# Kernel tuning notes

Measured on AMD Instinct MI355X. Metric: run time of the kernel, lower is better.

The kernel has to match this reference:

```python
import jax, jax.numpy as jnp
import numpy as np

N_HEADS = 16

def setup_inputs() -> dict:
    key = jax.random.key(0)
    ks = jax.random.split(key, 5)
    d = 2048
    s = 0.02
    return {
        "x": jax.random.normal(ks[0], (1, 2048, d), dtype=jnp.float32),
        "Wq": jax.random.normal(ks[1], (d, d), dtype=jnp.float32) * s,
        "bq": jnp.zeros((d,), jnp.float32),
        "Wk": jax.random.normal(ks[2], (d, d), dtype=jnp.float32) * s,
        "bk": jnp.zeros((d,), jnp.float32),
        "Wv": jax.random.normal(ks[3], (d, d), dtype=jnp.float32) * s,
        "bv": jnp.zeros((d,), jnp.float32),
        "Wo": jax.random.normal(ks[4], (d, d), dtype=jnp.float32) * s,
        "bo": jnp.zeros((d,), jnp.float32),
    }

def reference(x, Wq, bq, Wk, bk, Wv, bv, Wo, bo):
    B, S, D = x.shape
    H = N_HEADS
    dk = D // H
    # QKV projections -> [B, H, S, dk]
    def proj(W, b):
        return (x @ W + b).reshape(B, S, H, dk).transpose(0, 2, 1, 3)
    q, k, v = proj(Wq, bq), proj(Wk, bk), proj(Wv, bv)
    scores = jnp.einsum('bhqd,bhkd->bhqk', q, k) / jnp.sqrt(jnp.float32(dk))
    # _apply_sliding_window_attention: block-reshaped tril == plain causal mask
    causal = jnp.tril(jnp.ones((S, S), dtype=bool))
    scores = jnp.where(causal, scores, -jnp.inf)
    probs = jax.nn.softmax(scores, axis=-1)
    out = jnp.einsum('bhqk,bhkd->bhqd', probs, v)  # [B,H,S,dk]
    out = out.transpose(0, 2, 1, 3).reshape(B, S, D)
    return out @ Wo + bo
```

## Files before the change

kernel.cpp:

```cpp
#include <hip/hip_runtime.h>
#include <hip/hip_bf16.h>
#include <stdint.h>

typedef unsigned short u16;
typedef __attribute__((ext_vector_type(8))) __bf16 bf16x8;
typedef __attribute__((ext_vector_type(4))) float f32x4;

#define LOG2E 1.4426950408889634f

__device__ __forceinline__ float bf2f(u16 u) {
  union { uint32_t u; float f; } v; v.u = ((uint32_t)u) << 16;
  return v.f;
}

__device__ __forceinline__ uint32_t pk2(float a, float b) {
  union { __hip_bfloat162 h; uint32_t u; } x;
  x.h = __float22bfloat162_rn(make_float2(a, b));
  return x.u;
}

__device__ __forceinline__ void gl_lds16(const void* g, void* l) {
  __builtin_amdgcn_global_load_lds((const __attribute__((address_space(1))) void*)g,
                                   (__attribute__((address_space(3))) void*)l,
                                   16, 0, 0);
}

__device__ __forceinline__ f32x4 mfma16(bf16x8 a, bf16x8 b, f32x4 c) {
  return __builtin_amdgcn_mfma_f32_16x16x32_bf16(a, b, c, 0, 0, 0);
}

__global__ void cvt_bf16(const float* __restrict__ src, u16* __restrict__ dst) {
  int i = (blockIdx.x * 256 + threadIdx.x) * 4;
  float4 f = *(const float4*)(src + i);
  uint2 o;
  o.x = pk2(f.x, f.y);
  o.y = pk2(f.z, f.w);
  *(uint2*)(dst + i) = o;
}

__global__ void transpose_cvt(const float* __restrict__ W0, const float* __restrict__ W1,
                              const float* __restrict__ W2, const float* __restrict__ W3,
                              u16* __restrict__ out) {
  __shared__ float tile[64][65];
  int z = blockIdx.z;
  const float* W = (z == 0) ? W0 : (z == 1) ? W1 : (z == 2) ? W2 : W3;
  u16* dst = out + (size_t)z * 2048 * 2048;
  int k0 = blockIdx.y * 64, n0 = blockIdx.x * 64;
  int lx = threadIdx.x & 63, ly = threadIdx.x >> 6;
#pragma unroll
  for (int p = 0; p < 16; ++p) {
    int row = p * 4 + ly;
    tile[row][lx] = W[(size_t)(k0 + row) * 2048 + n0 + lx];
  }
  __syncthreads();
  int kc = threadIdx.x & 7;
  int rbase = threadIdx.x >> 3;
#pragma unroll
  for (int p = 0; p < 2; ++p) {
    int n = rbase + p * 32;
    uint4 o;
    o.x = pk2(tile[kc * 8 + 0][n], tile[kc * 8 + 1][n]);
    o.y = pk2(tile[kc * 8 + 2][n], tile[kc * 8 + 3][n]);
    o.z = pk2(tile[kc * 8 + 4][n], tile[kc * 8 + 5][n]);
    o.w = pk2(tile[kc * 8 + 6][n], tile[kc * 8 + 7][n]);
    *(uint4*)(dst + (size_t)(n0 + n) * 2048 + k0 + kc * 8) = o;
  }
}

__launch_bounds__(256, 2)
__global__ void gemm_bt(const u16* __restrict__ A, const u16* __restrict__ Bt,
                        const float* __restrict__ b0, const float* __restrict__ b1,
                        const float* __restrict__ b2,
                        u16* __restrict__ outQ, u16* __restrict__ outK,
                        u16* __restrict__ outVT) {
  extern __shared__ char smem[];
  u16* As = (u16*)smem;
  u16* Bs = (u16*)(smem + 16384);
  const int K = 2048;
  const int tid = threadIdx.x;
  const int lane = tid & 63, wid = tid >> 6;
  const int c = lane & 15, q = lane >> 4;
  const int wm = wid >> 1, wn = wid & 1;
  const int tm = blockIdx.y, tn = blockIdx.x;
  const size_t Abase = (size_t)tm * 128 * K;
  const size_t Bbase = (size_t)tn * 128 * K;

  f32x4 acc[4][4] = {};

  for (int kt = 0; kt < K / 64; ++kt) {
#pragma unroll
    for (int t = 0; t < 4; ++t) {
      int slot = wid * 256 + t * 64 + lane;
      int row = slot >> 3, cs = slot & 7;
      int cc = cs ^ (row & 7);
      const u16* ga = A + Abase + (size_t)row * K + kt * 64 + cc * 8;
      gl_lds16(ga, (char*)As + (size_t)(wid * 256 + t * 64) * 16);
      const u16* gb = Bt + Bbase + (size_t)row * K + kt * 64 + cc * 8;
      gl_lds16(gb, (char*)Bs + (size_t)(wid * 256 + t * 64) * 16);
    }
    __syncthreads();
#pragma unroll
    for (int kc = 0; kc < 2; ++kc) {
      bf16x8 af[4], bfr[4];
#pragma unroll
      for (int i = 0; i < 4; ++i) {
        int rowa = wm * 64 + i * 16 + c;
        int cha = ((kc << 2) | q) ^ (rowa & 7);
        af[i] = *(const bf16x8*)((const char*)As + rowa * 128 + cha * 16);
        int rowb = wn * 64 + i * 16 + c;
        int chb = ((kc << 2) | q) ^ (rowb & 7);
        bfr[i] = *(const bf16x8*)((const char*)Bs + rowb * 128 + chb * 16);
      }
#pragma unroll
      for (int i = 0; i < 4; ++i)
#pragma unroll
        for (int j = 0; j < 4; ++j)
          acc[i][j] = mfma16(af[i], bfr[j], acc[i][j]);
    }
    __syncthreads();
  }

  int proj = tn >> 4;
  int h = tn & 15;
  const float* bias = (proj == 0) ? b0 : (proj == 1) ? b1 : b2;
  if (proj < 2) {
    u16* out = (proj == 0) ? outQ : outK;
    float scale = (proj == 0) ? 0.08838834764831845f : 1.0f;
#pragma unroll
    for (int i = 0; i < 4; ++i) {
      int s0 = tm * 128 + wm * 64 + i * 16 + q * 4;
#pragma unroll
      for (int j = 0; j < 4; ++j) {
        int d = wn * 64 + j * 16 + c;
        float bv = bias[h * 128 + d];
        uint32_t p01 = pk2((acc[i][j][0] + bv) * scale, (acc[i][j][1] + bv) * scale);
        uint32_t p23 = pk2((acc[i][j][2] + bv) * scale, (acc[i][j][3] + bv) * scale);
        u16* o = out + ((size_t)h * 2048 + s0) * 128 + d;
        o[0]   = (u16)p01;
        o[128] = (u16)(p01 >> 16);
        o[256] = (u16)p23;
        o[384] = (u16)(p23 >> 16);
      }
    }
  } else {
    u16* Cs = (u16*)smem;
#pragma unroll
    for (int i = 0; i < 4; ++i) {
      int sl = wm * 64 + i * 16 + q * 4;
#pragma unroll
      for (int j = 0; j < 4; ++j) {
        int dl = wn * 64 + j * 16 + c;
        float bv = bias[h * 128 + dl];
        uint2 pk;
        pk.x = pk2(acc[i][j][0] + bv, acc[i][j][1] + bv);
        pk.y = pk2(acc[i][j][2] + bv, acc[i][j][3] + bv);
        *(uint2*)(Cs + dl * 136 + sl) = pk;
      }
    }
    __syncthreads();
#pragma unroll
    for (int rr = 0; rr < 8; ++rr) {
      int d = rr * 16 + (tid >> 4);
      int sc = (tid & 15) * 8;
      uint4 vv = *(const uint4*)(Cs + d * 136 + sc);
      *(uint4*)(outVT + ((size_t)(h * 128 + d)) * 2048 + tm * 128 + sc) = vv;
    }
  }
}

__launch_bounds__(256, 2)
__global__ void gemm_op(const u16* __restrict__ A, const u16* __restrict__ Bt,
                        const float* __restrict__ bias, float* __restrict__ out) {
  extern __shared__ char smem[];
  u16* As = (u16*)smem;
  u16* Bs = (u16*)(smem + 16384);
  const int K = 2048;
  const int tid = threadIdx.x;
  const int lane = tid & 63, wid = tid >> 6;
  const int c = lane & 15, q = lane >> 4;
  const int wm = wid >> 1, wn = wid & 1;
  const int tm = blockIdx.y, tn = blockIdx.x;
  const size_t Abase = (size_t)tm * 128 * K;
  const size_t Bbase = (size_t)tn * 64 * K;

  f32x4 acc[4][2] = {};

  for (int kt = 0; kt < K / 64; ++kt) {
#pragma unroll
    for (int t = 0; t < 4; ++t) {
      int slot = wid * 256 + t * 64 + lane;
      int row = slot >> 3, cs = slot & 7;
      int cc = cs ^ (row & 7);
      gl_lds16(A + Abase + (size_t)row * K + kt * 64 + cc * 8,
               (char*)As + (size_t)(wid * 256 + t * 64) * 16);
    }
#pragma unroll
    for (int t = 0; t < 2; ++t) {
      int slot = wid * 128 + t * 64 + lane;
      int row = slot >> 3, cs = slot & 7;
      int cc = cs ^ (row & 7);
      gl_lds16(Bt + Bbase + (size_t)row * K + kt * 64 + cc * 8,
               (char*)Bs + (size_t)(wid * 128 + t * 64) * 16);
    }
    __syncthreads();
#pragma unroll
    for (int kc = 0; kc < 2; ++kc) {
      bf16x8 af[4], bfr[2];
#pragma unroll
      for (int i = 0; i < 4; ++i) {
        int rowa = wm * 64 + i * 16 + c;
        int cha = ((kc << 2) | q) ^ (rowa & 7);
        af[i] = *(const bf16x8*)((const char*)As + rowa * 128 + cha * 16);
      }
#pragma unroll
      for (int j = 0; j < 2; ++j) {
        int rowb = wn * 32 + j * 16 + c;
        int chb = ((kc << 2) | q) ^ (rowb & 7);
        bfr[j] = *(const bf16x8*)((const char*)Bs + rowb * 128 + chb * 16);
      }
#pragma unroll
      for (int i = 0; i < 4; ++i)
#pragma unroll
        for (int j = 0; j < 2; ++j)
          acc[i][j] = mfma16(af[i], bfr[j], acc[i][j]);
    }
    __syncthreads();
  }

#pragma unroll
  for (int i = 0; i < 4; ++i) {
    int rowg = tm * 128 + wm * 64 + i * 16 + q * 4;
#pragma unroll
    for (int j = 0; j < 2; ++j) {
      int colg = tn * 64 + wn * 32 + j * 16 + c;
      float bv = bias[colg];
#pragma unroll
      for (int r = 0; r < 4; ++r)
        out[(size_t)(rowg + r) * 2048 + colg] = acc[i][j][r] + bv;
    }
  }
}

__launch_bounds__(256, 2)
__global__ void attn_kernel(const u16* __restrict__ Qb, const u16* __restrict__ Kb,
                            const u16* __restrict__ Vt,
                            u16* __restrict__ Opb, float* __restrict__ lpb) {
  extern __shared__ char smem[];
  u16* Ks = (u16*)smem;
  u16* Vs = (u16*)(smem + 16384);
  u16* Ps = (u16*)(smem + 32768);
  int b = blockIdx.x;
  int split, qt, h;
  if (b < 256) { split = 0; qt = b >> 4; h = b & 15; }
  else { split = 1; int idx = b - 256; qt = 15 - (idx >> 4); h = idx & 15; }
  u16* Op = Opb + (size_t)split * 4194304;
  float* lp = lpb + (size_t)split * 32768;
  const int ktBase = split ? (qt + 1) : 0;
  const int ntiles = qt + 1;

  const int tid = threadIdx.x, lane = tid & 63, wid = tid >> 6;
  const int c = lane & 15, q = lane >> 4;

  bf16x8 qf[2][4];
#pragma unroll
  for (int i = 0; i < 2; ++i) {
    int s = qt * 128 + wid * 32 + i * 16 + c;
    const u16* qrow = Qb + ((size_t)h * 2048 + s) * 128;
#pragma unroll
    for (int kc = 0; kc < 4; ++kc)
      qf[i][kc] = *(const bf16x8*)(qrow + kc * 32 + q * 8);
  }

  f32x4 oacc[2][8] = {};
  float lst[2][4] = {};

  for (int tt = 0; tt < ntiles; ++tt) {
    const int kt = ktBase + tt;
    if (tt) __syncthreads();
#pragma unroll
    for (int t = 0; t < 4; ++t) {
      int slot = (wid * 4 + t) * 64 + lane;
      int rowk = slot >> 4, csk = slot & 15;
      int cck = csk ^ (rowk & 7);
      const u16* gk = Kb + ((size_t)h * 2048 + kt * 64 + rowk) * 128 + cck * 8;
      gl_lds16(gk, (char*)Ks + (size_t)((wid * 4 + t) * 64) * 16);
      int rowv = slot >> 3, csv = slot & 7;
      int ccv = csv ^ (rowv & 7);
      const u16* gv = Vt + ((size_t)(h * 128 + rowv)) * 2048 + kt * 64 + ccv * 8;
      gl_lds16(gv, (char*)Vs + (size_t)((wid * 4 + t) * 64) * 16);
    }
    __syncthreads();

    f32x4 sacc[2][4] = {};
#pragma unroll
    for (int kc = 0; kc < 4; ++kc) {
      bf16x8 bfr[4];
#pragma unroll
      for (int j = 0; j < 4; ++j) {
        int row = j * 16 + c;
        int ch = ((kc << 2) | q) ^ (row & 7);
        bfr[j] = *(const bf16x8*)((const char*)Ks + row * 256 + ch * 16);
      }
#pragma unroll
      for (int i = 0; i < 2; ++i)
#pragma unroll
        for (int j = 0; j < 4; ++j)
          sacc[i][j] = mfma16(qf[i][kc], bfr[j], sacc[i][j]);
    }

    if (kt >= 2 * qt) {
#pragma unroll
      for (int i = 0; i < 2; ++i)
#pragma unroll
        for (int j = 0; j < 4; ++j) {
          int key = kt * 64 + j * 16 + c;
#pragma unroll
          for (int r = 0; r < 4; ++r) {
            int qrow = qt * 128 + wid * 32 + i * 16 + q * 4 + r;
            if (key > qrow) sacc[i][j][r] = -1e30f;
          }
        }
    }

#pragma unroll
    for (int i = 0; i < 2; ++i)
#pragma unroll
      for (int j = 0; j < 4; ++j)
#pragma unroll
        for (int r = 0; r < 4; ++r) {
          float p = __builtin_amdgcn_exp2f(sacc[i][j][r] * LOG2E);
          sacc[i][j][r] = p;
          lst[i][r] += p;
        }

#pragma unroll
    for (int i = 0; i < 2; ++i)
#pragma unroll
      for (int j = 0; j < 4; ++j) {
        uint32_t p01 = pk2(sacc[i][j][0], sacc[i][j][1]);
        uint32_t p23 = pk2(sacc[i][j][2], sacc[i][j][3]);
        u16* pp = Ps + wid * 2304 + (i * 16 + q * 4) * 72 + j * 16 + c;
        pp[0]   = (u16)p01;
        pp[72]  = (u16)(p01 >> 16);
        pp[144] = (u16)p23;
        pp[216] = (u16)(p23 >> 16);
      }

#pragma unroll
    for (int kc = 0; kc < 2; ++kc) {
      bf16x8 af[2], bv[8];
#pragma unroll
      for (int i = 0; i < 2; ++i)
        af[i] = *(const bf16x8*)((const char*)Ps + wid * 4608 + (i * 16 + c) * 144 +
                                 kc * 64 + q * 16);
#pragma unroll
      for (int jo = 0; jo < 8; ++jo) {
        int row = jo * 16 + c;
        int ch = ((kc << 2) | q) ^ (row & 7);
        bv[jo] = *(const bf16x8*)((const char*)Vs + row * 128 + ch * 16);
      }
#pragma unroll
      for (int i = 0; i < 2; ++i)
#pragma unroll
        for (int jo = 0; jo < 8; ++jo)
          oacc[i][jo] = mfma16(bv[jo], af[i], oacc[i][jo]);
    }
  }

#pragma unroll
  for (int i = 0; i < 2; ++i)
#pragma unroll
    for (int r = 0; r < 4; ++r) {
      float l = lst[i][r];
      l += __shfl_xor(l, 1);
      l += __shfl_xor(l, 2);
      l += __shfl_xor(l, 4);
      l += __shfl_xor(l, 8);
      if (c == 0)
        lp[(size_t)h * 2048 + qt * 128 + wid * 32 + i * 16 + q * 4 + r] = l;
    }
#pragma unroll
  for (int i = 0; i < 2; ++i) {
    int s = qt * 128 + wid * 32 + i * 16 + c;
#pragma unroll
    for (int jo = 0; jo < 8; ++jo) {
      uint2 o;
      o.x = pk2(oacc[i][jo][0], oacc[i][jo][1]);
      o.y = pk2(oacc[i][jo][2], oacc[i][jo][3]);
      *(uint2*)(Op + ((size_t)h * 2048 + s) * 128 + jo * 16 + q * 4) = o;
    }
  }
}

__global__ void attn_combine(const u16* __restrict__ Opb, const float* __restrict__ lpb,
                             u16* __restrict__ AO) {
  int g = blockIdx.x * 256 + threadIdx.x;
  int row = g >> 4;
  int dd = (g & 15) * 8;
  int h = row >> 11, s = row & 2047;
  float inv = 1.0f / (lpb[row] + lpb[row + 32768]);
  uint4 a = *(const uint4*)(Opb + (size_t)row * 128 + dd);
  uint4 bb = *(const uint4*)(Opb + 4194304 + (size_t)row * 128 + dd);
  const u16* pa = (const u16*)&a;
  const u16* pb = (const u16*)&bb;
  uint4 res;
  uint32_t* pr = (uint32_t*)&res;
#pragma unroll
  for (int t = 0; t < 4; ++t)
    pr[t] = pk2((bf2f(pa[2 * t]) + bf2f(pb[2 * t])) * inv,
                (bf2f(pa[2 * t + 1]) + bf2f(pb[2 * t + 1])) * inv);
  *(uint4*)(AO + (size_t)s * 2048 + h * 128 + dd) = res;
}

extern "C" void kernel_launch(void* const* d_in, const int* in_sizes, int n_in,
                              void* d_out, int out_size, void* d_ws, size_t ws_size,
                              hipStream_t stream) {
  const float* x  = (const float*)d_in[0];
  const float* Wq = (const float*)d_in[1];
  const float* bq = (const float*)d_in[2];
  const float* Wk = (const float*)d_in[3];
  const float* bk = (const float*)d_in[4];
  const float* Wv = (const float*)d_in[5];
  const float* bv = (const float*)d_in[6];
  const float* Wo = (const float*)d_in[7];
  const float* bo = (const float*)d_in[8];

  char* ws = (char*)d_ws;
  u16* xb = (u16*)(ws);
  u16* wt = (u16*)(ws + (size_t)8  * 1048576);
  u16* Qb = (u16*)(ws + (size_t)40 * 1048576);
  u16* Kb = (u16*)(ws + (size_t)48 * 1048576);
  u16* Vt = (u16*)(ws + (size_t)56 * 1048576);
  u16* AO = (u16*)(ws + (size_t)64 * 1048576);
  u16* Opb = (u16*)(ws);
  float* lpb = (float*)d_out;

  cvt_bf16<<<4096, 256, 0, stream>>>(x, xb);
  transpose_cvt<<<dim3(32, 32, 4), 256, 0, stream>>>(Wq, Wk, Wv, Wo, wt);
  gemm_bt<<<dim3(48, 16), 256, 34816, stream>>>(xb, wt, bq, bk, bv, Qb, Kb, Vt);
  attn_kernel<<<512, 256, 51200, stream>>>(Qb, Kb, Vt, Opb, lpb);
  attn_combine<<<2048, 256, 0, stream>>>(Opb, lpb, AO);
  gemm_op<<<dim3(32, 16), 256, 24576, stream>>>(AO, wt + (size_t)3 * 2048 * 2048,
                                                bo, (float*)d_out);
}
```

Before: 247.4 us.

## Fuse split-KV combine into attention via atomic flags and merge prep kernels

Merges the x conversion into the weight transpose/convert kernel as an extra grid slice, which removes one launch. The separate attn_combine kernel is dropped. Each (qtile, head) pair now uses an atomic counter, and whichever split block finishes second reads the other split's partial output and row sums. That block then writes the normalized result straight from its registers. This cuts one kernel launch and one full pass over the partial buffer, in exchange for threadfence/atomic cost and flags stored in the output buffer's scratch space.

```diff
diff --git a/kernel.cpp b/kernel.cpp
--- a/kernel.cpp
+++ b/kernel.cpp
@@ -29,22 +29,29 @@
   return __builtin_amdgcn_mfma_f32_16x16x32_bf16(a, b, c, 0, 0, 0);
 }
 
-__global__ void cvt_bf16(const float* __restrict__ src, u16* __restrict__ dst) {
-  int i = (blockIdx.x * 256 + threadIdx.x) * 4;
-  float4 f = *(const float4*)(src + i);
-  uint2 o;
-  o.x = pk2(f.x, f.y);
-  o.y = pk2(f.z, f.w);
-  *(uint2*)(dst + i) = o;
-}
-
-__global__ void transpose_cvt(const float* __restrict__ W0, const float* __restrict__ W1,
-                              const float* __restrict__ W2, const float* __restrict__ W3,
-                              u16* __restrict__ out) {
+__global__ void prep(const float* __restrict__ W0, const float* __restrict__ W1,
+                     const float* __restrict__ W2, const float* __restrict__ W3,
+                     u16* __restrict__ wt,
+                     const float* __restrict__ x, u16* __restrict__ xb,
+                     int* __restrict__ flags) {
+  int z = blockIdx.z;
+  if (z == 4) {
+    int bid = blockIdx.y * 32 + blockIdx.x;
+    if (bid == 0) flags[threadIdx.x] = 0;
+#pragma unroll
+    for (int k = 0; k < 4; ++k) {
+      int i = bid * 4096 + k * 1024 + threadIdx.x * 4;
+      float4 f = *(const float4*)(x + i);
+      uint2 o;
+      o.x = pk2(f.x, f.y);
+      o.y = pk2(f.z, f.w);
+      *(uint2*)(xb + i) = o;
+    }
+    return;
+  }
   __shared__ float tile[64][65];
-  int z = blockIdx.z;
   const float* W = (z == 0) ? W0 : (z == 1) ? W1 : (z == 2) ? W2 : W3;
-  u16* dst = out + (size_t)z * 2048 * 2048;
+  u16* dst = wt + (size_t)z * 2048 * 2048;
   int k0 = blockIdx.y * 64, n0 = blockIdx.x * 64;
   int lx = threadIdx.x & 63, ly = threadIdx.x >> 6;
 #pragma unroll
@@ -244,7 +251,8 @@
 __launch_bounds__(256, 2)
 __global__ void attn_kernel(const u16* __restrict__ Qb, const u16* __restrict__ Kb,
                             const u16* __restrict__ Vt,
-                            u16* __restrict__ Opb, float* __restrict__ lpb) {
+                            u16* __restrict__ Opb, float* __restrict__ lpb,
+                            int* __restrict__ flags, u16* __restrict__ AO) {
   extern __shared__ char smem[];
   u16* Ks = (u16*)smem;
   u16* Vs = (u16*)(smem + 16384);
@@ -367,6 +375,7 @@
     }
   }
 
+  float* lws = (float*)(smem + 32768) + wid * 32;
 #pragma unroll
   for (int i = 0; i < 2; ++i)
 #pragma unroll
@@ -376,8 +385,10 @@
       l += __shfl_xor(l, 2);
       l += __shfl_xor(l, 4);
       l += __shfl_xor(l, 8);
-      if (c == 0)
+      if (c == 0) {
         lp[(size_t)h * 2048 + qt * 128 + wid * 32 + i * 16 + q * 4 + r] = l;
+        lws[i * 16 + q * 4 + r] = l;
+      }
     }
 #pragma unroll
   for (int i = 0; i < 2; ++i) {
@@ -390,26 +401,35 @@
       *(uint2*)(Op + ((size_t)h * 2048 + s) * 128 + jo * 16 + q * 4) = o;
     }
   }
-}
-
-__global__ void attn_combine(const u16* __restrict__ Opb, const float* __restrict__ lpb,
-                             u16* __restrict__ AO) {
-  int g = blockIdx.x * 256 + threadIdx.x;
-  int row = g >> 4;
-  int dd = (g & 15) * 8;
-  int h = row >> 11, s = row & 2047;
-  float inv = 1.0f / (lpb[row] + lpb[row + 32768]);
-  uint4 a = *(const uint4*)(Opb + (size_t)row * 128 + dd);
-  uint4 bb = *(const uint4*)(Opb + 4194304 + (size_t)row * 128 + dd);
-  const u16* pa = (const u16*)&a;
-  const u16* pb = (const u16*)&bb;
-  uint4 res;
-  uint32_t* pr = (uint32_t*)&res;
-#pragma unroll
-  for (int t = 0; t < 4; ++t)
-    pr[t] = pk2((bf2f(pa[2 * t]) + bf2f(pb[2 * t])) * inv,
-                (bf2f(pa[2 * t + 1]) + bf2f(pb[2 * t + 1])) * inv);
-  *(uint4*)(AO + (size_t)s * 2048 + h * 128 + dd) = res;
+
+  __syncthreads();
+  int* sflag = (int*)(smem + 34816);
+  if (tid == 0) {
+    __threadfence();
+    *sflag = atomicAdd(&flags[qt * 16 + h], 1);
+  }
+  __syncthreads();
+  if (*sflag == 1) {
+    __threadfence();
+    const u16* Oo = Opb + (size_t)(1 - split) * 4194304;
+    const float* lo = lpb + (size_t)(1 - split) * 32768;
+#pragma unroll
+    for (int i = 0; i < 2; ++i) {
+      int s = qt * 128 + wid * 32 + i * 16 + c;
+      float inv = 1.0f / (lws[i * 16 + c] + lo[(size_t)h * 2048 + s]);
+#pragma unroll
+      for (int jo = 0; jo < 8; ++jo) {
+        uint2 ov = *(const uint2*)(Oo + ((size_t)h * 2048 + s) * 128 + jo * 16 + q * 4);
+        const u16* po = (const u16*)&ov;
+        uint2 res;
+        res.x = pk2((oacc[i][jo][0] + bf2f(po[0])) * inv,
+                    (oacc[i][jo][1] + bf2f(po[1])) * inv);
+        res.y = pk2((oacc[i][jo][2] + bf2f(po[2])) * inv,
+                    (oacc[i][jo][3] + bf2f(po[3])) * inv);
+        *(uint2*)(AO + (size_t)s * 2048 + h * 128 + jo * 16 + q * 4) = res;
+      }
+    }
+  }
 }
 
 extern "C" void kernel_launch(void* const* d_in, const int* in_sizes, int n_in,
@@ -434,12 +454,11 @@
   u16* AO = (u16*)(ws + (size_t)64 * 1048576);
   u16* Opb = (u16*)(ws);
   float* lpb = (float*)d_out;
-
-  cvt_bf16<<<4096, 256, 0, stream>>>(x, xb);
-  transpose_cvt<<<dim3(32, 32, 4), 256, 0, stream>>>(Wq, Wk, Wv, Wo, wt);
+  int* flags = (int*)((char*)d_out + 262144);
+
+  prep<<<dim3(32, 32, 5), 256, 0, stream>>>(Wq, Wk, Wv, Wo, wt, x, xb, flags);
   gemm_bt<<<dim3(48, 16), 256, 34816, stream>>>(xb, wt, bq, bk, bv, Qb, Kb, Vt);
-  attn_kernel<<<512, 256, 51200, stream>>>(Qb, Kb, Vt, Opb, lpb);
-  attn_combine<<<2048, 256, 0, stream>>>(Opb, lpb, AO);
+  attn_kernel<<<512, 256, 51200, stream>>>(Qb, Kb, Vt, Opb, lpb, flags, AO);
   gemm_op<<<dim3(32, 16), 256, 24576, stream>>>(AO, wt + (size_t)3 * 2048 * 2048,
                                                 bo, (float*)d_out);
 }
```

Measured after the change: 300.7 us. 1.22x slower.
